# Optimization experiments

Measured on AMD Instinct MI355X. Metric: run time of the kernel, lower is better.

The kernel has to match this reference:

```python
import jax, jax.numpy as jnp
import numpy as np
from jax import lax

D_MODEL = 512
D_STATE = 32
D_CONV = 4
D_INNER = 2 * D_MODEL
DT_RANK = (D_MODEL + 15) // 16  # 32
B_SZ, L = 8, 1024
EPS = 1e-12


def _mamba_params(key, pfx):
    ks = jax.random.split(key, 6)
    s = 0.02
    p = {}
    p[pfx + '_in_w'] = jax.random.normal(ks[0], (2 * D_INNER, D_MODEL)) * s
    p[pfx + '_conv_w'] = jax.random.normal(ks[1], (D_INNER, D_CONV)) * s
    p[pfx + '_conv_b'] = jnp.zeros((D_INNER,))
    p[pfx + '_xproj_w'] = jax.random.normal(ks[2], (DT_RANK + 2 * D_STATE, D_INNER)) * s
    p[pfx + '_dt_w'] = jax.random.normal(ks[3], (D_INNER, DT_RANK)) * s
    p[pfx + '_dt_b'] = jax.random.uniform(ks[4], (D_INNER,), minval=-4.0, maxval=-2.0)
    p[pfx + '_A_log'] = jnp.log(jnp.broadcast_to(jnp.arange(1, D_STATE + 1, dtype=jnp.float32), (D_INNER, D_STATE)))
    p[pfx + '_D'] = jnp.ones((D_INNER,))
    p[pfx + '_out_w'] = jax.random.normal(ks[5], (D_MODEL, D_INNER)) * s
    return p


def setup_inputs() -> dict:
    key = jax.random.key(0)
    ks = jax.random.split(key, 10)
    inp = {
        'hidden_states': jax.random.normal(ks[0], (B_SZ, L, D_MODEL)),
        'lengths': jax.random.randint(ks[1], (B_SZ,), 1, L + 1, dtype=jnp.int32),
    }
    inp.update(_mamba_params(ks[2], 'f'))
    inp.update(_mamba_params(ks[3], 'b'))
    s = 0.02
    inp['proj_w'] = jax.random.normal(ks[4], (1, 2)) * 0.5 + 0.5
    inp['proj_b'] = jnp.zeros((1,))
    inp['ln_g'] = jnp.ones((D_MODEL,))
    inp['ln_b'] = jnp.zeros((D_MODEL,))
    inp['ffn_w1'] = jax.random.normal(ks[5], (4 * D_MODEL, D_MODEL)) * s
    inp['ffn_b1'] = jnp.zeros((4 * D_MODEL,))
    inp['ffn_w2'] = jax.random.normal(ks[6], (D_MODEL, 4 * D_MODEL)) * s
    inp['ffn_b2'] = jnp.zeros((D_MODEL,))
    inp['ffn_ln_g'] = jnp.ones((D_MODEL,))
    inp['ffn_ln_b'] = jnp.zeros((D_MODEL,))
    return inp


def _layernorm(x, g, b):
    mu = jnp.mean(x, -1, keepdims=True)
    var = jnp.mean(jnp.square(x - mu), -1, keepdims=True)
    return (x - mu) * lax.rsqrt(var + EPS) * g + b


def _selective_scan(delta, Bm, Cm, u, A, D):
    # delta,u: (B,L,Di); Bm,Cm: (B,L,N); A: (Di,N); D: (Di,)
    def step(h, inp):
        d_t, B_t, C_t, u_t = inp
        dA = jnp.exp(d_t[..., None] * A)                 # (B,Di,N)
        h = dA * h + (d_t * u_t)[..., None] * B_t[:, None, :]
        y = jnp.einsum('bdn,bn->bd', h, C_t)
        return h, y
    h0 = jnp.zeros((u.shape[0], A.shape[0], A.shape[1]), u.dtype)
    xs = (delta.transpose(1, 0, 2), Bm.transpose(1, 0, 2),
          Cm.transpose(1, 0, 2), u.transpose(1, 0, 2))
    _, ys = lax.scan(step, h0, xs)
    return ys.transpose(1, 0, 2) + u * D


def _mamba(x, in_w, conv_w, conv_b, xproj_w, dt_w, dt_b, A_log, Dp, out_w):
    xz = jnp.einsum('bld,ed->ble', x, in_w)              # (B,L,2Di)
    x_in, z = jnp.split(xz, 2, axis=-1)
    # causal depthwise conv1d
    xc = jnp.pad(x_in.transpose(0, 2, 1), ((0, 0), (0, 0), (D_CONV - 1, 0)))
    xc = lax.conv_general_dilated(xc, conv_w[:, None, :], (1,), 'VALID',
                                  dimension_numbers=('NCH', 'OIH', 'NCH'),
                                  feature_group_count=D_INNER)
    xc = jax.nn.silu(xc + conv_b[None, :, None]).transpose(0, 2, 1)  # (B,L,Di)
    x_dbl = jnp.einsum('bld,ed->ble', xc, xproj_w)
    dt, Bm, Cm = jnp.split(x_dbl, [DT_RANK, DT_RANK + D_STATE], axis=-1)
    delta = jax.nn.softplus(jnp.einsum('blr,dr->bld', dt, dt_w) + dt_b)
    A = -jnp.exp(A_log)
    y = _selective_scan(delta, Bm, Cm, xc, A, Dp)
    y = y * jax.nn.silu(z)
    return jnp.einsum('bld,ed->ble', y, out_w)


def reference(hidden_states, lengths,
              f_in_w, f_conv_w, f_conv_b, f_xproj_w, f_dt_w, f_dt_b, f_A_log, f_D, f_out_w,
              b_in_w, b_conv_w, b_conv_b, b_xproj_w, b_dt_w, b_dt_b, b_A_log, b_D, b_out_w,
              proj_w, proj_b, ln_g, ln_b,
              ffn_w1, ffn_b1, ffn_w2, ffn_b2, ffn_ln_g, ffn_ln_b):
    x = hidden_states
    hf = _mamba(x, f_in_w, f_conv_w, f_conv_b, f_xproj_w, f_dt_w, f_dt_b, f_A_log, f_D, f_out_w)
    hb = _mamba(jnp.flip(x, 1), b_in_w, b_conv_w, b_conv_b, b_xproj_w, b_dt_w, b_dt_b, b_A_log, b_D, b_out_w)
    hb = jnp.flip(hb, 1)
    # Linear(2,1) over stacked [hf,hb] on last axis
    out = hf * proj_w[0, 0] + hb * proj_w[0, 1] + proj_b[0]
    out1 = _layernorm(out + x, ln_g, ln_b)  # dropout = identity (eval)
    h = jax.nn.gelu(jnp.einsum('bld,ed->ble', out1, ffn_w1) + ffn_b1, approximate=False)
    h = jnp.einsum('ble,de->bld', h, ffn_w2) + ffn_b2
    return _layernorm(h + out1, ffn_ln_g, ffn_ln_b)
```

## Files before the change

### kernel.cpp

```cpp
#include <hip/hip_runtime.h>
#include <hip/hip_bf16.h>
#include <hip/hip_fp16.h>
#include <math.h>

typedef __hip_bfloat16 bf16;
typedef __attribute__((ext_vector_type(8))) short bfrag;
typedef __attribute__((ext_vector_type(4))) float ffrag;
typedef __attribute__((ext_vector_type(4))) float f4;
typedef __attribute__((ext_vector_type(4))) short sh4;

#define BSZ    8
#define LSEQ   1024
#define DMODEL 512
#define DINNER 1024
#define DSTATE 32
#define DTRANK 32
#define MROWS  (BSZ * LSEQ)

__device__ __forceinline__ float bf2f(bf16 v) { return __bfloat162float(v); }
__device__ __forceinline__ float s2f(short s) {
    union { unsigned u; float f; } c; c.u = ((unsigned)(unsigned short)s) << 16; return c.f;
}
__device__ __forceinline__ short f2s(float v) {
    union { bf16 b; short s; } u; u.b = __float2bfloat16(v); return u.s;
}
__device__ __forceinline__ void stC(float* p, size_t i, float v) { p[i] = v; }
__device__ __forceinline__ void stC(bf16* p, size_t i, float v) { p[i] = __float2bfloat16(v); }
__device__ __forceinline__ float fsigmoid(float x) {
    return __builtin_amdgcn_rcpf(1.f + __expf(-x));
}
__device__ __forceinline__ float fexp2(float x) { return __builtin_amdgcn_exp2f(x); }

__device__ __forceinline__ float dload(const void* p, size_t i, int f) {
    if (f == 1) return ((const float*)p)[i];
    if (f == 2) return __half2float(((const __half*)p)[i]);
    if (f == 3) return (float)((const double*)p)[i];
    return bf2f(((const bf16*)p)[i]);
}

enum { ACT_NONE = 0, ACT_SOFTPLUS = 1, ACT_GELU = 2 };

__global__ void resolve_kernel(const void* a8, const void* d9, const void* d22,
                               const void* s0, const void* s1, int* flags)
{
    if (blockIdx.x != 0) return;
    const int lane = threadIdx.x;
    const int cand[4] = {1, 0, 2, 3};
    int fw = -1;
    for (int ci = 0; ci < 4 && fw < 0; ++ci) {
        int f = cand[ci];
        bool ok = true;
        if (lane < 48) {
            float e = logf((float)((lane & 31) + 1));
            float v = dload(a8, lane, f);
            ok = (v == v) && fabsf(v - e) <= 0.02f * e + 0.02f;
        } else if (lane < 56) {
            int k = lane - 48;
            ok = fabsf(dload(d9, k, f) - 1.f) <= 0.01f &&
                 fabsf(dload(d22, k, f) - 1.f) <= 0.01f;
        }
        if (__all(ok)) fw = f;
    }
    int fx = -1, xs = -1;
    for (int si = 0; si < 2 && fx < 0; ++si) {
        const void* p = (si == 0) ? s0 : s1;
        for (int ci = 0; ci < 4 && fx < 0; ++ci) {
            int f = cand[ci];
            bool ok = true;
            float s = 0.f, s2 = 0.f;
            for (int k = lane; k < 256; k += 64) {
                float v = dload(p, k, f);
                ok = ok && (v == v) && fabsf(v) < 16.f;
                s += v; s2 += v * v;
            }
            int allok = __all(ok);
            for (int m = 1; m < 64; m <<= 1) {
                s += __shfl_xor(s, m); s2 += __shfl_xor(s2, m);
            }
            if (allok) {
                float mu = s * (1.f / 256.f);
                float var = s2 * (1.f / 256.f) - mu * mu;
                if (var > 0.25f && var < 4.f) { fx = f; xs = si; }
            }
        }
    }
    if (lane == 0) {
        flags[0] = (fw < 0) ? 1 : fw;
        flags[1] = (fx < 0) ? 1 : fx;
        flags[2] = (xs < 0) ? 0 : xs;
        flags[3] = (fw == 1 && fx == 1) ? 1 : 0;
    }
}

__global__ __launch_bounds__(256) void cvt_x_kernel(const void* x0, const void* x1,
                                                    bf16* __restrict__ dst,
                                                    const int* __restrict__ flags)
{
    const void* x = flags[2] ? x1 : x0;
    const int fx = flags[1];
    int i = blockIdx.x * 256 + threadIdx.x;
    if (fx == 1) {
        f4 v = ((const f4*)x)[i];
        sh4 o;
#pragma unroll
        for (int j = 0; j < 4; ++j) o[j] = f2s(v[j]);
        ((sh4*)dst)[i] = o;
    } else {
#pragma unroll
        for (int j = 0; j < 4; ++j)
            dst[(size_t)i * 4 + j] = __float2bfloat16(dload(x, (size_t)i * 4 + j, fx));
    }
}

__global__ __launch_bounds__(256) void cvt3_kernel(
    const float* __restrict__ s0, bf16* __restrict__ d0, int n0,
    const float* __restrict__ s1, bf16* __restrict__ d1, int n1,
    const float* __restrict__ s2, bf16* __restrict__ d2, int n2)
{
    int i = blockIdx.x * 256 + threadIdx.x;
    const float* s; bf16* d; int off;
    if (i < n0) { s = s0; d = d0; off = i; }
    else if (i < n0 + n1) { s = s1; d = d1; off = i - n0; }
    else if (i < n0 + n1 + n2) { s = s2; d = d2; off = i - n0 - n1; }
    else return;
    f4 v = ((const f4*)s)[off];
    sh4 o;
#pragma unroll
    for (int j = 0; j < 4; ++j) o[j] = f2s(v[j]);
    ((sh4*)d)[off] = o;
}

__global__ __launch_bounds__(256) void transpose_kernel(
    const bf16* __restrict__ src, bf16* __restrict__ dst, int R, int D)
{
    __shared__ short t[64][72];
    const int r0 = blockIdx.x * 64, d0 = blockIdx.y * 64;
    const int tr = threadIdx.x >> 3;
    const int tc = (threadIdx.x & 7) * 8;
#pragma unroll
    for (int h = 0; h < 2; ++h) {
        int d = tr + h * 32;
        bfrag v = *(const bfrag*)&src[(size_t)(d0 + d) * R + r0 + tc];
#pragma unroll
        for (int j = 0; j < 8; ++j) t[tc + j][d] = v[j];
    }
    __syncthreads();
#pragma unroll
    for (int h = 0; h < 2; ++h) {
        int r = tr + h * 32;
        bfrag v = *(const bfrag*)&t[r][tc];
        *(bfrag*)&dst[(size_t)(r0 + r) * D + d0 + tc] = v;
    }
}

__global__ __launch_bounds__(256) void conv8_kernel(
    const bf16* __restrict__ xin_T,
    const void* __restrict__ cw, const void* __restrict__ cb,
    bf16* __restrict__ u_T,
    const int* __restrict__ flags)
{
    const int fw = flags[0];
    int blk = blockIdx.x;
    int chunk = blk & 3;
    int d = blk >> 2;
    int m = chunk * 2048 + threadIdx.x * 8;
    size_t base = (size_t)d * MROWS;
    float w0 = dload(cw, d * 4 + 0, fw), w1 = dload(cw, d * 4 + 1, fw);
    float w2 = dload(cw, d * 4 + 2, fw), w3 = dload(cw, d * 4 + 3, fw);
    float cbv = dload(cb, d, fw);
    const bf16* src = &xin_T[base + m];
    bfrag v = *(const bfrag*)src;
    float x[11];
    if (m & (LSEQ - 1)) {
        bfrag pv = *(const bfrag*)(src - 8);
        x[0] = s2f(pv[5]); x[1] = s2f(pv[6]); x[2] = s2f(pv[7]);
    } else { x[0] = 0.f; x[1] = 0.f; x[2] = 0.f; }
#pragma unroll
    for (int j = 0; j < 8; ++j) x[3 + j] = s2f(v[j]);
    bfrag o;
#pragma unroll
    for (int j = 0; j < 8; ++j) {
        float a = cbv + x[j] * w0 + x[j + 1] * w1 + x[j + 2] * w2 + x[j + 3] * w3;
        a = a * fsigmoid(a);
        o[j] = f2s(a);
    }
    *(bfrag*)&u_T[base + m] = o;
}

__device__ __forceinline__ void glds16(const bf16* g, short* l)
{
    __builtin_amdgcn_global_load_lds(
        (const __attribute__((address_space(1))) void*)g,
        (__attribute__((address_space(3))) void*)l,
        16, 0, 0);
}

template <int FLIPB, int ACT, typename CT>
__global__ __launch_bounds__(256) void bgemm_kernel(
    const bf16* __restrict__ A, int lda,
    const bf16* __restrict__ B, int ldb,
    const float* __restrict__ bias,
    CT* __restrict__ C, int ldc, int K)
{
    __shared__ __align__(16) short As[2][128 * 32];
    __shared__ __align__(16) short Bs[2][128 * 32];
    const int tid = threadIdx.x;
    const int bm = blockIdx.y * 128, bn = blockIdx.x * 128;
    const int lane = tid & 63, w = tid >> 6;

    const int srow = lane >> 2;
    const int skc  = (lane & 3) << 3;
    const int arow0 = bm + w * 32 + srow;
    int brow0 = bn + w * 32 + srow;
    int brow1 = brow0 + 16;
    if (FLIPB) {
        brow0 = (brow0 & ~(LSEQ - 1)) + (LSEQ - 1 - (brow0 & (LSEQ - 1)));
        brow1 = (brow1 & ~(LSEQ - 1)) + (LSEQ - 1 - (brow1 & (LSEQ - 1)));
    }
    const bf16* ga0 = A + (size_t)arow0 * lda + skc;
    const bf16* ga1 = ga0 + (size_t)16 * lda;
    const bf16* gb0 = B + (size_t)brow0 * ldb + skc;
    const bf16* gb1 = B + (size_t)brow1 * ldb + skc;
    const int lA0 = (w * 32) * 32, lA1 = (w * 32 + 16) * 32;

    const int wm = (w & 1) << 6, wn = (w >> 1) << 6;
    const int lm = lane & 15, quad = lane >> 4;

    ffrag acc[4][4];
#pragma unroll
    for (int i = 0; i < 4; ++i)
#pragma unroll
        for (int j = 0; j < 4; ++j)
#pragma unroll
            for (int e = 0; e < 4; ++e) acc[i][j][e] = 0.f;

    glds16(ga0, &As[0][lA0]);
    glds16(ga1, &As[0][lA1]);
    glds16(gb0, &Bs[0][lA0]);
    glds16(gb1, &Bs[0][lA1]);
    __syncthreads();

    int cur = 0;
    for (int k0 = 0; k0 < K; k0 += 32) {
        if (k0 + 32 < K) {
            glds16(ga0 + k0 + 32, &As[cur ^ 1][lA0]);
            glds16(ga1 + k0 + 32, &As[cur ^ 1][lA1]);
            glds16(gb0 + k0 + 32, &Bs[cur ^ 1][lA0]);
            glds16(gb1 + k0 + 32, &Bs[cur ^ 1][lA1]);
        }
        bfrag af[4], bfv[4];
#pragma unroll
        for (int ti = 0; ti < 4; ++ti)
            af[ti] = *(const bfrag*)&As[cur][(wm + ti * 16 + lm) * 32 + quad * 8];
#pragma unroll
        for (int tj = 0; tj < 4; ++tj)
            bfv[tj] = *(const bfrag*)&Bs[cur][(wn + tj * 16 + lm) * 32 + quad * 8];
#pragma unroll
        for (int ti = 0; ti < 4; ++ti)
#pragma unroll
            for (int tj = 0; tj < 4; ++tj)
                acc[ti][tj] = __builtin_amdgcn_mfma_f32_16x16x32_bf16(
                    af[ti], bfv[tj], acc[ti][tj], 0, 0, 0);
        __syncthreads();
        cur ^= 1;
    }

#pragma unroll
    for (int tj = 0; tj < 4; ++tj) {
        int col = bn + wn + tj * 16 + lm;
        float bcv = bias ? bias[col] : 0.f;
#pragma unroll
        for (int ti = 0; ti < 4; ++ti) {
#pragma unroll
            for (int r2 = 0; r2 < 4; ++r2) {
                int rowg = bm + wm + ti * 16 + quad * 4 + r2;
                float v = acc[ti][tj][r2] + bcv;
                if (ACT == ACT_GELU) v = 0.5f * v * (1.f + erff(v * 0.70710678118654752f));
                stC(C, (size_t)rowg * ldc + col, v);
            }
        }
    }
}

template <int ACT, int XPROJ, int RES, typename CT>
__global__ __launch_bounds__(256) void bgemm64_kernel(
    const bf16* __restrict__ A, int lda,
    const bf16* __restrict__ B, int ldb,
    const float* __restrict__ bias,
    CT* __restrict__ C, int ldc,
    float* __restrict__ C2,
    const bf16* __restrict__ res,
    int M, int K)
{
    __shared__ __align__(16) short As[2][128 * 64];
    __shared__ __align__(16) short Bs[2][64 * 64];
    const int tid = threadIdx.x;
    const int bm = blockIdx.y * 128, bn = blockIdx.x * 64;
    const int lane = tid & 63, w = tid >> 6;

    const int lr = lane >> 3;
    const int sc = ((lane & 7) ^ lr) << 3;

    const bf16* ga[4];
#pragma unroll
    for (int a = 0; a < 4; ++a) {
        int ar = bm + w * 32 + a * 8 + lr;
        if (ar >= M) ar = M - 1;
        ga[a] = A + (size_t)ar * lda + sc;
    }
    const bf16* gb[2];
#pragma unroll
    for (int a = 0; a < 2; ++a) {
        int br = bn + w * 16 + a * 8 + lr;
        gb[a] = B + (size_t)br * ldb + sc;
    }
    const int lA = (w * 32) * 64, lB = (w * 16) * 64;

    const int wm = (w & 1) << 6, wn = (w >> 1) << 5;
    const int lm = lane & 15, quad = lane >> 4;

    ffrag acc[4][2];
#pragma unroll
    for (int i = 0; i < 4; ++i)
#pragma unroll
        for (int j = 0; j < 2; ++j)
#pragma unroll
            for (int e = 0; e < 4; ++e) acc[i][j][e] = 0.f;

#pragma unroll
    for (int a = 0; a < 4; ++a) glds16(ga[a], &As[0][lA + a * 8 * 64]);
#pragma unroll
    for (int a = 0; a < 2; ++a) glds16(gb[a], &Bs[0][lB + a * 8 * 64]);
    __syncthreads();

    int cur = 0;
    for (int k0 = 0; k0 < K; k0 += 64) {
        if (k0 + 64 < K) {
#pragma unroll
            for (int a = 0; a < 4; ++a) glds16(ga[a] + k0 + 64, &As[cur ^ 1][lA + a * 8 * 64]);
#pragma unroll
            for (int a = 0; a < 2; ++a) glds16(gb[a] + k0 + 64, &Bs[cur ^ 1][lB + a * 8 * 64]);
        }
        bfrag af[2][4], bfv[2][2];
#pragma unroll
        for (int kk = 0; kk < 2; ++kk) {
#pragma unroll
            for (int ti = 0; ti < 4; ++ti) {
                int row = wm + ti * 16 + lm;
                int c = kk * 4 + quad;
                af[kk][ti] = *(const bfrag*)&As[cur][row * 64 + ((c ^ (row & 7)) << 3)];
            }
#pragma unroll
            for (int tj = 0; tj < 2; ++tj) {
                int row = wn + tj * 16 + lm;
                int c = kk * 4 + quad;
                bfv[kk][tj] = *(const bfrag*)&Bs[cur][row * 64 + ((c ^ (row & 7)) << 3)];
            }
        }
#pragma unroll
        for (int kk = 0; kk < 2; ++kk)
#pragma unroll
            for (int ti = 0; ti < 4; ++ti)
#pragma unroll
                for (int tj = 0; tj < 2; ++tj)
                    acc[ti][tj] = __builtin_amdgcn_mfma_f32_16x16x32_bf16(
                        af[kk][ti], bfv[kk][tj], acc[ti][tj], 0, 0, 0);
        __syncthreads();
        cur ^= 1;
    }

#pragma unroll
    for (int tj = 0; tj < 2; ++tj) {
        int col = bn + wn + tj * 16 + lm;
        float bcv = bias ? bias[col] : 0.f;
#pragma unroll
        for (int ti = 0; ti < 4; ++ti) {
#pragma unroll
            for (int r2 = 0; r2 < 4; ++r2) {
                int rowg = bm + wm + ti * 16 + quad * 4 + r2;
                if (XPROJ) {
                    float v = acc[ti][tj][r2];
                    if (rowg < 32)
                        ((float*)C)[(size_t)rowg * ldc + col] = v;
                    else if (rowg < 96)
                        C2[(((size_t)col >> 3) * 64 + (rowg - 32)) * 8 + (col & 7)] = v;
                } else if (rowg < M) {
                    float v = acc[ti][tj][r2] + bcv;
                    if (ACT == ACT_GELU) v = 0.5f * v * (1.f + erff(v * 0.70710678118654752f));
                    if (RES) v += bf2f(res[(size_t)rowg * ldc + col]);
                    stC(C, (size_t)rowg * ldc + col, v);
                }
            }
        }
    }
}

__global__ __launch_bounds__(256) void dt_kernel(
    const float* __restrict__ xdT,
    const float* __restrict__ dt_w,
    const float* __restrict__ dt_b,
    bf16* __restrict__ delta_T)
{
    const int m = blockIdx.x * 256 + threadIdx.x;
    const int d0 = blockIdx.y * 64;
    float v[32];
#pragma unroll
    for (int r = 0; r < 32; ++r) v[r] = xdT[(size_t)r * MROWS + m];
    for (int d = d0; d < d0 + 64; ++d) {
        float acc = dt_b[d];
#pragma unroll
        for (int r = 0; r < 32; ++r) acc = fmaf(dt_w[d * 32 + r], v[r], acc);
        acc = (acc > 20.f) ? acc : log1pf(__expf(acc));
        delta_T[(size_t)d * MROWS + m] = __float2bfloat16(acc);
    }
}

#define SCH 8
struct ScanBuf { float dl[SCH], uv[SCH], Bv[SCH], Cv[SCH]; float zsc, usc; };

__device__ __forceinline__ void scan_load(ScanBuf& s,
    const bf16* __restrict__ dT, const bf16* __restrict__ uT,
    const bf16* __restrict__ zT, const float* __restrict__ xm,
    size_t lb, int coff, int n)
{
    bfrag dv = *(const bfrag*)&dT[lb];
    bfrag uv = *(const bfrag*)&uT[lb];
#pragma unroll
    for (int j = 0; j < SCH; ++j) { s.dl[j] = s2f(dv[j]); s.uv[j] = s2f(uv[j]); }
    s.zsc = bf2f(zT[lb + (n & 7)]);
    s.usc = bf2f(uT[lb + (n & 7)]);
    const float* bp = xm + coff + n * 8;
    f4 b0 = *(const f4*)bp;
    f4 b1 = *(const f4*)(bp + 4);
    const float* cp = bp + 256;
    f4 c0 = *(const f4*)cp;
    f4 c1 = *(const f4*)(cp + 4);
#pragma unroll
    for (int j = 0; j < 4; ++j) {
        s.Bv[j] = b0[j]; s.Bv[4 + j] = b1[j];
        s.Cv[j] = c0[j]; s.Cv[4 + j] = c1[j];
    }
}

__device__ __forceinline__ void scan_compute(const ScanBuf& s, float& h,
    float Ad2, float Dd, bf16* __restrict__ yT, size_t lb,
    bool b0, bool b1, bool b2, bool wr)
{
    float p[SCH];
#pragma unroll
    for (int j = 0; j < SCH; ++j) {
        float dlv = s.dl[j];
        h = fexp2(dlv * Ad2) * h + dlv * s.uv[j] * s.Bv[j];
        p[j] = h * s.Cv[j];
    }
    float q[4];
#pragma unroll
    for (int jj = 0; jj < 4; ++jj) {
        float keep = b0 ? p[2 * jj + 1] : p[2 * jj];
        float send = b0 ? p[2 * jj] : p[2 * jj + 1];
        q[jj] = keep + __shfl_xor(send, 1);
    }
    float r0 = (b1 ? q[1] : q[0]) + __shfl_xor(b1 ? q[0] : q[1], 2);
    float r1 = (b1 ? q[3] : q[2]) + __shfl_xor(b1 ? q[2] : q[3], 2);
    float t = (b2 ? r1 : r0) + __shfl_xor(b2 ? r0 : r1, 4);
    t += __shfl_xor(t, 8);
    t += __shfl_xor(t, 16);
    if (wr) {
        float y = t + s.usc * Dd;
        float g = s.zsc;
        y *= g * fsigmoid(g);
        yT[lb + (threadIdx.x & 7)] = __float2bfloat16(y);
    }
}

__global__ __launch_bounds__(256) void scan_kernel(
    const bf16* __restrict__ delta_T,
    bf16* __restrict__ u_T,
    const bf16* __restrict__ z_T,
    const float* __restrict__ xdbl_m,
    const void* __restrict__ A_log,
    const void* __restrict__ Dp,
    const int* __restrict__ flags)
{
    const int fw = flags[0];
    const int tid = threadIdx.x;
    const int n = tid & 31;
    const int dloc = tid >> 5;
    const int gd = blockIdx.x * 8 + dloc;
    const int b = gd >> 10;
    const int d = gd & (DINNER - 1);
    const bool b0 = n & 1, b1 = n & 2, b2 = n & 4;
    const bool wr = (n < 8);

    const float Ad2 = -__expf(dload(A_log, d * DSTATE + n, fw)) * 1.44269504088896341f;
    const float Dd = dload(Dp, d, fw);
    const size_t lbase = (size_t)d * MROWS + b * LSEQ;
    const float* xmb = xdbl_m + ((size_t)b * LSEQ >> 3) * 512;
    float h = 0.f;

    ScanBuf bufA, bufB;
    scan_load(bufA, delta_T, u_T, z_T, xmb, lbase, 0, n);
    for (int c0 = 0; c0 < LSEQ / SCH; c0 += 2) {
        scan_load(bufB, delta_T, u_T, z_T, xmb,
                  lbase + (size_t)(c0 + 1) * SCH, (c0 + 1) * 512, n);
        scan_compute(bufA, h, Ad2, Dd, u_T, lbase + (size_t)c0 * SCH, b0, b1, b2, wr);
        if (c0 + 2 < LSEQ / SCH)
            scan_load(bufA, delta_T, u_T, z_T, xmb,
                      lbase + (size_t)(c0 + 2) * SCH, (c0 + 2) * 512, n);
        scan_compute(bufB, h, Ad2, Dd, u_T, lbase + (size_t)(c0 + 1) * SCH, b0, b1, b2, wr);
    }
}

__global__ __launch_bounds__(256) void combine_ln_kernel(
    const bf16* __restrict__ hf, const bf16* __restrict__ hb,
    const void* __restrict__ x0, const void* __restrict__ x1,
    const void* __restrict__ pw, const void* __restrict__ pb,
    const void* __restrict__ g, const void* __restrict__ be,
    bf16* __restrict__ out1,
    const int* __restrict__ flags)
{
    const int fw = flags[0];
    const int fx = flags[1];
    const void* x = flags[2] ? x1 : x0;
    const int lane = threadIdx.x & 63;
    int row = blockIdx.x * 4 + (threadIdx.x >> 6);
    int b = row >> 10, l = row & (LSEQ - 1);
    int rrow = (b << 10) + (LSEQ - 1 - l);
    float pw0 = dload(pw, 0, fw), pw1 = dload(pw, 1, fw), pbv = dload(pb, 0, fw);
    int c0 = lane * 8;
    bfrag hfv = *(const bfrag*)&hf[(size_t)row * DMODEL + c0];
    bfrag hbv = *(const bfrag*)&hb[(size_t)rrow * DMODEL + c0];
    float v[8], s = 0.f, s2 = 0.f;
#pragma unroll
    for (int j = 0; j < 8; ++j) {
        float val = s2f(hfv[j]) * pw0 + s2f(hbv[j]) * pw1 + pbv
                  + dload(x, (size_t)row * DMODEL + c0 + j, fx);
        v[j] = val; s += val; s2 += val * val;
    }
#pragma unroll
    for (int m = 1; m < 64; m <<= 1) { s += __shfl_xor(s, m); s2 += __shfl_xor(s2, m); }
    float mu = s * (1.f / DMODEL);
    float var = s2 * (1.f / DMODEL) - mu * mu;
    float r = rsqrtf(fmaxf(var, 0.f) + 1e-12f);
    bfrag o;
#pragma unroll
    for (int j = 0; j < 8; ++j)
        o[j] = f2s((v[j] - mu) * r * dload(g, c0 + j, fw) + dload(be, c0 + j, fw));
    *(bfrag*)&out1[(size_t)row * DMODEL + c0] = o;
}

__global__ __launch_bounds__(256) void final_ln_kernel(
    const float* __restrict__ out2,
    const void* __restrict__ g, const void* __restrict__ be,
    float* __restrict__ out,
    const int* __restrict__ flags)
{
    const int fw = flags[0];
    const int valid = flags[3];
    const int lane = threadIdx.x & 63;
    int row = blockIdx.x * 4 + (threadIdx.x >> 6);
    int c0 = lane * 8;
    f4 a0 = *(const f4*)&out2[(size_t)row * DMODEL + c0];
    f4 a1 = *(const f4*)&out2[(size_t)row * DMODEL + c0 + 4];
    float v[8], s = 0.f, s2 = 0.f;
#pragma unroll
    for (int j = 0; j < 4; ++j) { v[j] = a0[j]; v[4 + j] = a1[j]; }
#pragma unroll
    for (int j = 0; j < 8; ++j) { s += v[j]; s2 += v[j] * v[j]; }
#pragma unroll
    for (int m = 1; m < 64; m <<= 1) { s += __shfl_xor(s, m); s2 += __shfl_xor(s2, m); }
    float mu = s * (1.f / DMODEL);
    float var = s2 * (1.f / DMODEL) - mu * mu;
    float r = rsqrtf(fmaxf(var, 0.f) + 1e-12f);
    f4 o0, o1;
#pragma unroll
    for (int j = 0; j < 8; ++j) {
        float val = (v[j] - mu) * r * dload(g, c0 + j, fw) + dload(be, c0 + j, fw);
        val = valid ? val : 0.f;
        if (j < 4) o0[j] = val; else o1[j - 4] = val;
    }
    *(f4*)&out[(size_t)row * DMODEL + c0] = o0;
    *(f4*)&out[(size_t)row * DMODEL + c0 + 4] = o1;
}

extern "C" void kernel_launch(void* const* d_in, const int* in_sizes, int n_in,
                              void* d_out, int out_size, void* d_ws, size_t ws_size,
                              hipStream_t stream)
{
    const void* x0 = d_in[0];
    const void* x1 = d_in[1];
    const void* proj_w   = d_in[20];
    const void* proj_b   = d_in[21];
    const void* ln_g     = d_in[22];
    const void* ln_b     = d_in[23];
    const float* ffn_w1  = (const float*)d_in[24];
    const float* ffn_b1  = (const float*)d_in[25];
    const float* ffn_w2  = (const float*)d_in[26];
    const float* ffn_b2  = (const float*)d_in[27];
    const void* ffn_ln_g = d_in[28];
    const void* ffn_ln_b = d_in[29];

    char* wsb = (char*)d_ws;
    char* ob  = (char*)d_out;
    bf16*  xin_T   = (bf16*)(wsb + 0);
    bf16*  z_T     = (bf16*)(wsb + (16u << 20));
    bf16*  uy_T    = (bf16*)(wsb + (32u << 20));
    bf16*  u_rm    = (bf16*)(wsb + 0);
    bf16*  delta_T = (bf16*)(wsb + 0);
    bf16*  y_rm    = (bf16*)(wsb + 0);
    float* xdT     = (float*)(wsb + (48u << 20));
    bf16*  in_w_bf = (bf16*)(wsb + (51u << 20));
    float* xdbl_m  = (float*)(wsb + (51u << 20));
    bf16*  xp_w_bf = (bf16*)(wsb + (53u << 20));
    bf16*  o_w_bf  = (bf16*)(wsb + (54u << 20));
    bf16*  hf      = (bf16*)d_out;
    bf16*  hb      = (bf16*)d_out + (size_t)MROWS * DMODEL;
    bf16*  xbf     = (bf16*)(ob + (8u << 20));
    bf16*  w1bf    = (bf16*)(ob + 0);
    bf16*  w2bf    = (bf16*)(ob + (2u << 20));
    bf16*  out1    = (bf16*)(wsb + 0);
    bf16*  ffn_h   = (bf16*)(wsb + (8u << 20));
    float* out2    = (float*)(wsb + (40u << 20));
    int*   flags   = (int*)(wsb + (56u << 20));

    dim3 blk(256);

    resolve_kernel<<<dim3(1), dim3(64), 0, stream>>>(
        d_in[8], d_in[9], d_in[22], x0, x1, flags);
    cvt_x_kernel<<<dim3(4096), blk, 0, stream>>>(x0, x1, xbf, flags);

    for (int dir = 0; dir < 2; ++dir) {
        int pb0 = 2 + dir * 9;
        const float* in_w    = (const float*)d_in[pb0 + 0];
        const void*  conv_w  = d_in[pb0 + 1];
        const void*  conv_b  = d_in[pb0 + 2];
        const float* xproj_w = (const float*)d_in[pb0 + 3];
        const float* dt_w    = (const float*)d_in[pb0 + 4];
        const float* dt_b    = (const float*)d_in[pb0 + 5];
        const void*  A_log   = d_in[pb0 + 6];
        const void*  Dp      = d_in[pb0 + 7];
        const float* out_w   = (const float*)d_in[pb0 + 8];
        bf16* hout = (dir == 0) ? hf : hb;

        cvt3_kernel<<<dim3(1632), blk, 0, stream>>>(
            in_w, in_w_bf, (2048 * 512) / 4,
            xproj_w, xp_w_bf, (96 * 1024) / 4,
            out_w, o_w_bf, (512 * 1024) / 4);

        if (dir == 0)
            bgemm_kernel<0, ACT_NONE, bf16><<<dim3(64, 16), blk, 0, stream>>>(
                in_w_bf, DMODEL, xbf, DMODEL, nullptr, xin_T, MROWS, DMODEL);
        else
            bgemm_kernel<1, ACT_NONE, bf16><<<dim3(64, 16), blk, 0, stream>>>(
                in_w_bf, DMODEL, xbf, DMODEL, nullptr, xin_T, MROWS, DMODEL);

        conv8_kernel<<<dim3(DINNER * 4), blk, 0, stream>>>(
            xin_T, conv_w, conv_b, uy_T, flags);
        transpose_kernel<<<dim3(128, 16), blk, 0, stream>>>(uy_T, u_rm, MROWS, DINNER);
        bgemm64_kernel<ACT_NONE, 1, 0, float><<<dim3(128, 1), blk, 0, stream>>>(
            xp_w_bf, DINNER, u_rm, DINNER, nullptr,
            xdT, MROWS, xdbl_m, nullptr, 96, DINNER);
        dt_kernel<<<dim3(32, 16), blk, 0, stream>>>(xdT, dt_w, dt_b, delta_T);
        scan_kernel<<<dim3((BSZ * DINNER) / 8), blk, 0, stream>>>(
            delta_T, uy_T, z_T, xdbl_m, A_log, Dp, flags);
        transpose_kernel<<<dim3(128, 16), blk, 0, stream>>>(uy_T, y_rm, MROWS, DINNER);
        bgemm64_kernel<ACT_NONE, 0, 0, bf16><<<dim3(8, 64), blk, 0, stream>>>(
            y_rm, DINNER, o_w_bf, DINNER, nullptr, hout, DMODEL, nullptr, nullptr,
            MROWS, DINNER);
    }

    combine_ln_kernel<<<dim3(MROWS / 4), blk, 0, stream>>>(
        hf, hb, x0, x1, proj_w, proj_b, ln_g, ln_b, out1, flags);
    cvt3_kernel<<<dim3(2048), blk, 0, stream>>>(
        ffn_w1, w1bf, (2048 * 512) / 4,
        ffn_w2, w2bf, (512 * 2048) / 4,
        nullptr, nullptr, 0);
    bgemm_kernel<0, ACT_GELU, bf16><<<dim3(16, 64), blk, 0, stream>>>(
        out1, DMODEL, w1bf, DMODEL, ffn_b1, ffn_h, 2048, DMODEL);
    bgemm64_kernel<ACT_NONE, 0, 1, float><<<dim3(8, 64), blk, 0, stream>>>(
        ffn_h, 2048, w2bf, 2048, ffn_b2, out2, DMODEL, nullptr, out1,
        MROWS, 2048);
    final_ln_kernel<<<dim3(MROWS / 4), blk, 0, stream>>>(
        out2, ffn_ln_g, ffn_ln_b, (float*)d_out, flags);
}
```

Baseline: 827.0 us.

## Keep two K-tiles of global-to-LDS loads in flight in GEMM main loops

Both GEMM kernels now issue loads for two K-stages up front and use explicit vmcnt waits plus raw s_barrier and sched_barrier. The load for stage k+2 is issued into the buffer just consumed, replacing the single-prefetch-then-__syncthreads pattern. This lets global loads overlap more compute and avoids the full-drain waits that __syncthreads implies. It relies on hand-counted vmcnt values that must match the number of outstanding glds16 ops, and on K being at least two tiles.

```diff
diff --git a/kernel.cpp b/kernel.cpp
--- a/kernel.cpp
+++ b/kernel.cpp
@@ -234,36 +234,50 @@
 #pragma unroll
             for (int e = 0; e < 4; ++e) acc[i][j][e] = 0.f;
 
-    glds16(ga0, &As[0][lA0]);
-    glds16(ga1, &As[0][lA1]);
-    glds16(gb0, &Bs[0][lA0]);
-    glds16(gb1, &Bs[0][lA1]);
-    __syncthreads();
-
+#define BG_STAGE(buf, kk)                      \
+    do {                                       \
+        glds16(ga0 + (kk), &As[buf][lA0]);     \
+        glds16(ga1 + (kk), &As[buf][lA1]);     \
+        glds16(gb0 + (kk), &Bs[buf][lA0]);     \
+        glds16(gb1 + (kk), &Bs[buf][lA1]);     \
+    } while (0)
+
+#define BG_COMPUTE(buf)                                                        \
+    do {                                                                       \
+        bfrag af[4], bfv[4];                                                   \
+        _Pragma("unroll")                                                      \
+        for (int ti = 0; ti < 4; ++ti)                                         \
+            af[ti] = *(const bfrag*)&As[buf][(wm + ti * 16 + lm) * 32 + quad * 8]; \
+        _Pragma("unroll")                                                      \
+        for (int tj = 0; tj < 4; ++tj)                                         \
+            bfv[tj] = *(const bfrag*)&Bs[buf][(wn + tj * 16 + lm) * 32 + quad * 8]; \
+        _Pragma("unroll")                                                      \
+        for (int ti = 0; ti < 4; ++ti)                                         \
+            _Pragma("unroll")                                                  \
+            for (int tj = 0; tj < 4; ++tj)                                     \
+                acc[ti][tj] = __builtin_amdgcn_mfma_f32_16x16x32_bf16(         \
+                    af[ti], bfv[tj], acc[ti][tj], 0, 0, 0);                    \
+    } while (0)
+
+    BG_STAGE(0, 0);
+    BG_STAGE(1, 32);
     int cur = 0;
-    for (int k0 = 0; k0 < K; k0 += 32) {
-        if (k0 + 32 < K) {
-            glds16(ga0 + k0 + 32, &As[cur ^ 1][lA0]);
-            glds16(ga1 + k0 + 32, &As[cur ^ 1][lA1]);
-            glds16(gb0 + k0 + 32, &Bs[cur ^ 1][lA0]);
-            glds16(gb1 + k0 + 32, &Bs[cur ^ 1][lA1]);
-        }
-        bfrag af[4], bfv[4];
-#pragma unroll
-        for (int ti = 0; ti < 4; ++ti)
-            af[ti] = *(const bfrag*)&As[cur][(wm + ti * 16 + lm) * 32 + quad * 8];
-#pragma unroll
-        for (int tj = 0; tj < 4; ++tj)
-            bfv[tj] = *(const bfrag*)&Bs[cur][(wn + tj * 16 + lm) * 32 + quad * 8];
-#pragma unroll
-        for (int ti = 0; ti < 4; ++ti)
-#pragma unroll
-            for (int tj = 0; tj < 4; ++tj)
-                acc[ti][tj] = __builtin_amdgcn_mfma_f32_16x16x32_bf16(
-                    af[ti], bfv[tj], acc[ti][tj], 0, 0, 0);
-        __syncthreads();
+    for (int k0 = 0; k0 < K - 32; k0 += 32) {
+        asm volatile("s_waitcnt vmcnt(4)" ::: "memory");
+        __builtin_amdgcn_s_barrier();
+        __builtin_amdgcn_sched_barrier(0);
+        BG_COMPUTE(cur);
+        __builtin_amdgcn_s_barrier();
+        __builtin_amdgcn_sched_barrier(0);
+        if (k0 + 64 < K) BG_STAGE(cur, k0 + 64);
         cur ^= 1;
     }
+    asm volatile("s_waitcnt vmcnt(0)" ::: "memory");
+    __builtin_amdgcn_s_barrier();
+    __builtin_amdgcn_sched_barrier(0);
+    BG_COMPUTE(cur);
+#undef BG_STAGE
+#undef BG_COMPUTE
 
 #pragma unroll
     for (int tj = 0; tj < 4; ++tj) {
@@ -327,47 +341,63 @@
 #pragma unroll
             for (int e = 0; e < 4; ++e) acc[i][j][e] = 0.f;
 
-#pragma unroll
-    for (int a = 0; a < 4; ++a) glds16(ga[a], &As[0][lA + a * 8 * 64]);
-#pragma unroll
-    for (int a = 0; a < 2; ++a) glds16(gb[a], &Bs[0][lB + a * 8 * 64]);
-    __syncthreads();
-
+#define BG64_STAGE(buf, kk)                                              \
+    do {                                                                 \
+        _Pragma("unroll")                                                \
+        for (int a = 0; a < 4; ++a)                                      \
+            glds16(ga[a] + (kk), &As[buf][lA + a * 8 * 64]);             \
+        _Pragma("unroll")                                                \
+        for (int a = 0; a < 2; ++a)                                      \
+            glds16(gb[a] + (kk), &Bs[buf][lB + a * 8 * 64]);             \
+    } while (0)
+
+#define BG64_COMPUTE(buf)                                                      \
+    do {                                                                       \
+        bfrag af[2][4], bfv[2][2];                                             \
+        _Pragma("unroll")                                                      \
+        for (int kk = 0; kk < 2; ++kk) {                                       \
+            _Pragma("unroll")                                                  \
+            for (int ti = 0; ti < 4; ++ti) {                                   \
+                int row = wm + ti * 16 + lm;                                   \
+                int c = kk * 4 + quad;                                         \
+                af[kk][ti] = *(const bfrag*)&As[buf][row * 64 + ((c ^ (row & 7)) << 3)]; \
+            }                                                                  \
+            _Pragma("unroll")                                                  \
+            for (int tj = 0; tj < 2; ++tj) {                                   \
+                int row = wn + tj * 16 + lm;                                   \
+                int c = kk * 4 + quad;                                         \
+                bfv[kk][tj] = *(const bfrag*)&Bs[buf][row * 64 + ((c ^ (row & 7)) << 3)]; \
+            }                                                                  \
+        }                                                                      \
+        _Pragma("unroll")                                                      \
+        for (int kk = 0; kk < 2; ++kk)                                         \
+            _Pragma("unroll")                                                  \
+            for (int ti = 0; ti < 4; ++ti)                                     \
+                _Pragma("unroll")                                              \
+                for (int tj = 0; tj < 2; ++tj)                                 \
+                    acc[ti][tj] = __builtin_amdgcn_mfma_f32_16x16x32_bf16(     \
+                        af[kk][ti], bfv[kk][tj], acc[ti][tj], 0, 0, 0);        \
+    } while (0)
+
+    BG64_STAGE(0, 0);
+    BG64_STAGE(1, 64);
     int cur = 0;
-    for (int k0 = 0; k0 < K; k0 += 64) {
-        if (k0 + 64 < K) {
-#pragma unroll
-            for (int a = 0; a < 4; ++a) glds16(ga[a] + k0 + 64, &As[cur ^ 1][lA + a * 8 * 64]);
-#pragma unroll
-            for (int a = 0; a < 2; ++a) glds16(gb[a] + k0 + 64, &Bs[cur ^ 1][lB + a * 8 * 64]);
-        }
-        bfrag af[2][4], bfv[2][2];
-#pragma unroll
-        for (int kk = 0; kk < 2; ++kk) {
-#pragma unroll
-            for (int ti = 0; ti < 4; ++ti) {
-                int row = wm + ti * 16 + lm;
-                int c = kk * 4 + quad;
-                af[kk][ti] = *(const bfrag*)&As[cur][row * 64 + ((c ^ (row & 7)) << 3)];
-            }
-#pragma unroll
-            for (int tj = 0; tj < 2; ++tj) {
-                int row = wn + tj * 16 + lm;
-                int c = kk * 4 + quad;
-                bfv[kk][tj] = *(const bfrag*)&Bs[cur][row * 64 + ((c ^ (row & 7)) << 3)];
-            }
-        }
-#pragma unroll
-        for (int kk = 0; kk < 2; ++kk)
-#pragma unroll
-            for (int ti = 0; ti < 4; ++ti)
-#pragma unroll
-                for (int tj = 0; tj < 2; ++tj)
-                    acc[ti][tj] = __builtin_amdgcn_mfma_f32_16x16x32_bf16(
-                        af[kk][ti], bfv[kk][tj], acc[ti][tj], 0, 0, 0);
-        __syncthreads();
+    for (int k0 = 0; k0 < K - 64; k0 += 64) {
+        asm volatile("s_waitcnt vmcnt(6)" ::: "memory");
+        __builtin_amdgcn_s_barrier();
+        __builtin_amdgcn_sched_barrier(0);
+        BG64_COMPUTE(cur);
+        __builtin_amdgcn_s_barrier();
+        __builtin_amdgcn_sched_barrier(0);
+        if (k0 + 128 < K) BG64_STAGE(cur, k0 + 128);
         cur ^= 1;
     }
+    asm volatile("s_waitcnt vmcnt(0)" ::: "memory");
+    __builtin_amdgcn_s_barrier();
+    __builtin_amdgcn_sched_barrier(0);
+    BG64_COMPUTE(cur);
+#undef BG64_STAGE
+#undef BG64_COMPUTE
 
 #pragma unroll
     for (int tj = 0; tj < 2; ++tj) {
```

Result: no change. 812.8 us (-1.7%).
